# Performance work log

Hardware: AMD Instinct MI355X
Metric: run time of the kernel (lower is better)

## Reference

```python
import jax, jax.numpy as jnp
import numpy as np

N = 100000   # nodes
E = 1000000  # edges
G = 5000     # graphs
IN = 64; H = 64; ED = 16; OUT = 1
NUM_LAYERS = 3; NUM_TIMESTEPS = 2
SLOPE = 0.01

if NUM_LAYERS >= NUM_TIMESTEPS:
    CACHED_INDEX = list(range(-NUM_TIMESTEPS, 0))
else:
    CACHED_INDEX = list(range(-NUM_LAYERS, 0)) + [-1] * (NUM_TIMESTEPS - NUM_LAYERS)


def leaky(x):
    return jnp.where(x > 0, x, SLOPE * x)


def seg_softmax(scores, index, num_segments):
    # scores: [E] edge scores, softmax within segments given by index (PyG softmax, +1e-16 denom)
    m = jax.ops.segment_max(scores, index, num_segments)
    m = jnp.where(jnp.isfinite(m), m, 0.0)
    e = jnp.exp(scores - m[index])
    s = jax.ops.segment_sum(e, index, num_segments)
    return e / (s[index] + 1e-16)


def gru_cell(x, h, wih, whh, bih, bhh):
    # torch.nn.GRUCell math
    gi = x @ wih.T + bih
    gh = h @ whh.T + bhh
    ir, iz, inn = jnp.split(gi, 3, axis=-1)
    hr, hz, hn = jnp.split(gh, 3, axis=-1)
    r = jax.nn.sigmoid(ir + hr)
    z = jax.nn.sigmoid(iz + hz)
    n = jnp.tanh(inn + r * hn)
    return (1.0 - z) * n + z * h


def setup_inputs() -> dict:
    key = jax.random.key(0)
    ks = jax.random.split(key, 32)
    f32 = jnp.float32
    def w(k, shape, fan_in):
        return jax.random.normal(k, shape, f32) * (1.0 / np.sqrt(fan_in))
    L2 = NUM_LAYERS - 1
    inp = {}
    inp['raw'] = jax.random.normal(ks[0], (N, IN), f32)
    inp['edge_index'] = jax.random.randint(ks[1], (2, E), 0, N)
    inp['edge_attr'] = jax.random.normal(ks[2], (E, ED), f32)
    inp['batch'] = jnp.sort(jax.random.randint(ks[3], (N,), 0, G))
    inp['lin1_w'] = w(ks[4], (H, IN), IN); inp['lin1_b'] = jnp.zeros((H,), f32)
    inp['gate_nl_w'] = w(ks[5], (H, IN + ED), IN + ED); inp['gate_nl_b'] = jnp.zeros((H,), f32)
    inp['gate_align_w'] = w(ks[6], (1, 2 * H), 2 * H); inp['gate_align_b'] = jnp.zeros((1,), f32)
    inp['gate_attend_w'] = w(ks[7], (H, H), H); inp['gate_attend_b'] = jnp.zeros((H,), f32)
    inp['conv_align_w'] = w(ks[8], (L2, 1, 2 * H), 2 * H); inp['conv_align_b'] = jnp.zeros((L2, 1), f32)
    inp['conv_attend_w'] = w(ks[9], (L2, H, H), H); inp['conv_attend_b'] = jnp.zeros((L2, H), f32)
    inp['atom_gru_wih'] = w(ks[10], (NUM_LAYERS, 3 * H, H), H)
    inp['atom_gru_whh'] = w(ks[11], (NUM_LAYERS, 3 * H, H), H)
    inp['atom_gru_bih'] = jnp.zeros((NUM_LAYERS, 3 * H), f32)
    inp['atom_gru_bhh'] = jnp.zeros((NUM_LAYERS, 3 * H), f32)
    inp['mol_align_w'] = w(ks[12], (1, 2 * H), 2 * H); inp['mol_align_b'] = jnp.zeros((1,), f32)
    inp['mol_attend_w'] = w(ks[13], (H, H), H); inp['mol_attend_b'] = jnp.zeros((H,), f32)
    inp['mol_gru_wih'] = w(ks[14], (3 * H, H), H)
    inp['mol_gru_whh'] = w(ks[15], (3 * H, H), H)
    inp['mol_gru_bih'] = jnp.zeros((3 * H,), f32)
    inp['mol_gru_bhh'] = jnp.zeros((3 * H,), f32)
    inp['lin2_w'] = w(ks[16], (OUT, H), H); inp['lin2_b'] = jnp.zeros((OUT,), f32)
    return inp


def reference(raw, edge_index, edge_attr, batch,
              lin1_w, lin1_b,
              gate_nl_w, gate_nl_b, gate_align_w, gate_align_b, gate_attend_w, gate_attend_b,
              conv_align_w, conv_align_b, conv_attend_w, conv_attend_b,
              atom_gru_wih, atom_gru_whh, atom_gru_bih, atom_gru_bhh,
              mol_align_w, mol_align_b, mol_attend_w, mol_attend_b,
              mol_gru_wih, mol_gru_whh, mol_gru_bih, mol_gru_bhh,
              lin2_w, lin2_b):
    src, dst = edge_index[0], edge_index[1]
    x = leaky(raw @ lin1_w.T + lin1_b)  # [N, H]

    # --- GATEConv (layer 0): x_j from raw, x_i from x ---
    xj = leaky(jnp.concatenate([raw[src], edge_attr], axis=-1) @ gate_nl_w.T + gate_nl_b)  # [E, H]
    score = leaky(jnp.concatenate([x[dst], xj], axis=-1) @ gate_align_w.T + gate_align_b)  # [E, 1]
    aw = seg_softmax(score[:, 0], dst, N)[:, None]
    msg = (xj @ gate_attend_w.T + gate_attend_b) * aw
    h = jax.nn.elu(jax.ops.segment_sum(msg, dst, N))
    x = jax.nn.relu(gru_cell(h, x, atom_gru_wih[0], atom_gru_whh[0], atom_gru_bih[0], atom_gru_bhh[0]))
    cached = [x]

    # --- GATConv layers 1..L-1 ---
    for l in range(NUM_LAYERS - 1):
        xi, xj = x[dst], x[src]
        score = leaky(jnp.concatenate([xi, xj], axis=-1) @ conv_align_w[l].T + conv_align_b[l])
        aw = seg_softmax(score[:, 0], dst, N)[:, None]
        msg = (xj @ conv_attend_w[l].T + conv_attend_b[l]) * aw
        h = jax.nn.elu(jax.ops.segment_sum(msg, dst, N))
        x = jax.nn.relu(gru_cell(h, x, atom_gru_wih[l + 1], atom_gru_whh[l + 1],
                                 atom_gru_bih[l + 1], atom_gru_bhh[l + 1]))
        cached.append(x)

    # --- molecule-level readout ---
    out = jax.nn.relu(jax.ops.segment_sum(x, batch, G))  # [G, H]
    for t in range(NUM_TIMESTEPS):
        mixed = (x + cached[CACHED_INDEX[t]]) * 0.5  # [N, H] (x_j); x_i = out[batch]
        score = leaky(jnp.concatenate([out[batch], mixed], axis=-1) @ mol_align_w.T + mol_align_b)
        aw = seg_softmax(score[:, 0], batch, G)[:, None]
        msg = (mixed @ mol_attend_w.T + mol_attend_b) * aw
        h = jax.nn.elu(jax.ops.segment_sum(msg, batch, G))
        out = jax.nn.relu(gru_cell(h, out, mol_gru_wih, mol_gru_whh, mol_gru_bih, mol_gru_bhh))

    return out @ lin2_w.T + lin2_b  # [G, OUT]
```

## Files before the change

kernel.cpp:

```cpp
#include <hip/hip_runtime.h>
#include <math.h>

#define NPAD 65

__device__ __forceinline__ float leaky(float x) { return x > 0.f ? x : 0.01f * x; }
__device__ __forceinline__ float eluf(float x)  { return x > 0.f ? x : (__expf(x) - 1.f); }
__device__ __forceinline__ float sigm(float x)  { return 1.f / (1.f + __expf(-x)); }
__device__ __forceinline__ float tanhfast(float x) { return 1.f - 2.f / (__expf(2.f * x) + 1.f); }

__device__ __forceinline__ float bcastf(float v, int k) {
    return __uint_as_float((unsigned)__builtin_amdgcn_readlane((int)__float_as_uint(v), k));
}
__device__ __forceinline__ int bcasti(int v, int k) {
    return __builtin_amdgcn_readlane(v, k);
}
__device__ __forceinline__ float wredsum(float v) {
    #pragma unroll
    for (int off = 32; off; off >>= 1) v += __shfl_xor(v, off);
    return v;
}
__device__ __forceinline__ float wredmax(float v) {
    #pragma unroll
    for (int off = 32; off; off >>= 1) v = fmaxf(v, __shfl_xor(v, off));
    return v;
}

__global__ __launch_bounds__(256) void k_hist(const int* __restrict__ ei, int* __restrict__ deg, int E_) {
    int e = blockIdx.x * 256 + threadIdx.x;
    if (e < E_) atomicAdd(&deg[ei[E_ + e]], 1);
}

__global__ __launch_bounds__(256) void k_scan1(const int* __restrict__ deg, int* __restrict__ bsum, int N_) {
    __shared__ int s[256];
    int i = blockIdx.x * 256 + threadIdx.x;
    s[threadIdx.x] = (i < N_) ? deg[i] : 0;
    __syncthreads();
    for (int off = 128; off; off >>= 1) {
        if (threadIdx.x < off) s[threadIdx.x] += s[threadIdx.x + off];
        __syncthreads();
    }
    if (threadIdx.x == 0) bsum[blockIdx.x] = s[0];
}

__global__ __launch_bounds__(512) void k_scan2(int* __restrict__ bsum, int nb) {
    __shared__ int s[512];
    __shared__ int carry_s;
    if (threadIdx.x == 0) carry_s = 0;
    __syncthreads();
    for (int base = 0; base < nb; base += 512) {
        int t = threadIdx.x;
        int idx = base + t;
        int v = (idx < nb) ? bsum[idx] : 0;
        s[t] = v;
        __syncthreads();
        #pragma unroll
        for (int off = 1; off < 512; off <<= 1) {
            int u = (t >= off) ? s[t - off] : 0;
            __syncthreads();
            s[t] += u;
            __syncthreads();
        }
        int carry = carry_s;
        if (idx < nb) bsum[idx] = carry + s[t] - v;
        __syncthreads();
        if (t == 0) carry_s = carry + s[511];
        __syncthreads();
    }
}

__global__ __launch_bounds__(256) void k_scan3(const int* __restrict__ deg, const int* __restrict__ bsum,
                                               int* __restrict__ row, int* __restrict__ cur, int N_, int E_) {
    __shared__ int s[256];
    int i = blockIdx.x * 256 + threadIdx.x;
    int d = (i < N_) ? deg[i] : 0;
    s[threadIdx.x] = d;
    __syncthreads();
    for (int off = 1; off < 256; off <<= 1) {
        int v = (threadIdx.x >= off) ? s[threadIdx.x - off] : 0;
        __syncthreads();
        s[threadIdx.x] += v;
        __syncthreads();
    }
    if (i < N_) {
        int ex = bsum[blockIdx.x] + s[threadIdx.x] - d;
        row[i] = ex; cur[i] = ex;
    }
    if (i == N_ - 1) row[N_] = E_;
}

__global__ __launch_bounds__(256) void k_scatter(const int* __restrict__ ei, int* __restrict__ cur,
                                                 int* __restrict__ csrc, int* __restrict__ ceid, int E_) {
    int e = blockIdx.x * 256 + threadIdx.x;
    if (e >= E_) return;
    int dst = ei[E_ + e];
    int slot = atomicAdd(&cur[dst], 1);
    csrc[slot] = ei[e];
    ceid[slot] = e;
}

__global__ __launch_bounds__(256) void k_gbounds(const int* __restrict__ batch, int* __restrict__ gst,
                                                 int N_, int G_) {
    int i = blockIdx.x * 256 + threadIdx.x;
    if (i >= N_) return;
    int b = batch[i];
    int prev = (i == 0) ? -1 : batch[i - 1];
    for (int g = prev + 1; g <= b; ++g) gst[g] = i;
    if (i == N_ - 1) { for (int g = b + 1; g <= G_; ++g) gst[g] = N_; }
}

__global__ __launch_bounds__(256) void k_dense64(
    const float* __restrict__ in, const float* __restrict__ w, int wstride,
    const float* __restrict__ b, float* __restrict__ outp, int M, int act)
{
    __shared__ float ti[64 * NPAD];
    __shared__ float to[64 * NPAD];
    int r0 = blockIdx.x * 64;
    for (int i = threadIdx.x; i < 4096; i += 256) {
        int r = i >> 6, c = i & 63; int gr = r0 + r;
        ti[r * NPAD + c] = (gr < M) ? in[(size_t)gr * 64 + c] : 0.f;
    }
    __syncthreads();
    int n = threadIdx.x & 63;
    int jl = __builtin_amdgcn_readfirstlane((threadIdx.x >> 6) << 4);
    float acc[16];
    #pragma unroll
    for (int jj = 0; jj < 16; ++jj) acc[jj] = b[jl + jj];
    for (int kc = 0; kc < 64; kc += 16) {
        float xr[16];
        #pragma unroll
        for (int i = 0; i < 16; ++i) xr[i] = ti[n * NPAD + kc + i];
        #pragma unroll
        for (int jj = 0; jj < 16; ++jj) {
            const float* wr = w + (jl + jj) * wstride + kc;
            #pragma unroll
            for (int i = 0; i < 16; ++i) acc[jj] = fmaf(wr[i], xr[i], acc[jj]);
        }
    }
    #pragma unroll
    for (int jj = 0; jj < 16; ++jj) {
        float v = acc[jj];
        to[n * NPAD + jl + jj] = act ? leaky(v) : v;
    }
    __syncthreads();
    for (int i = threadIdx.x; i < 4096; i += 256) {
        int r = i >> 6, c = i & 63; int gr = r0 + r;
        if (gr < M) outp[(size_t)gr * 64 + c] = to[r * NPAD + c];
    }
}

__global__ __launch_bounds__(256) void k_node_dot2(
    const float* __restrict__ x, const float* __restrict__ wa,
    const float* __restrict__ wb, float* __restrict__ s,
    float* __restrict__ t, int n, int two)
{
    int gt = blockIdx.x * 256 + threadIdx.x;
    int wid = gt >> 6, lane = threadIdx.x & 63;
    if (wid >= n) return;
    float xv = x[(size_t)wid * 64 + lane];
    float a = xv * wa[lane];
    float bb = two ? xv * wb[lane] : 0.f;
    #pragma unroll
    for (int off = 32; off; off >>= 1) {
        a  += __shfl_down(a, off);
        bb += __shfl_down(bb, off);
    }
    if (lane == 0) { s[wid] = a; if (two) t[wid] = bb; }
}

#define GDOT(acc, A0, A1, A2, A3) \
    acc = fmaf(A0.x, w2[0], acc);  acc = fmaf(A0.y, w2[1], acc);  \
    acc = fmaf(A0.z, w2[2], acc);  acc = fmaf(A0.w, w2[3], acc);  \
    acc = fmaf(A1.x, w2[4], acc);  acc = fmaf(A1.y, w2[5], acc);  \
    acc = fmaf(A1.z, w2[6], acc);  acc = fmaf(A1.w, w2[7], acc);  \
    acc = fmaf(A2.x, w2[8], acc);  acc = fmaf(A2.y, w2[9], acc);  \
    acc = fmaf(A2.z, w2[10], acc); acc = fmaf(A2.w, w2[11], acc); \
    acc = fmaf(A3.x, w2[12], acc); acc = fmaf(A3.y, w2[13], acc); \
    acc = fmaf(A3.z, w2[14], acc); acc = fmaf(A3.w, w2[15], acc);

__global__ __launch_bounds__(256, 4) void k_gate_gather(
    const float* __restrict__ u, const float* __restrict__ ea,
    const int* __restrict__ row, const int* __restrict__ csrc, const int* __restrict__ ceid,
    const float* __restrict__ wnl,
    const float* __restrict__ gaw, const float* __restrict__ gab,
    const float* __restrict__ sarr, float* __restrict__ Agg, int N_)
{
    int wid = (blockIdx.x * 256 + threadIdx.x) >> 6;
    int lane = threadIdx.x & 63;
    if (wid >= N_) return;
    float w2[16];
    #pragma unroll
    for (int k = 0; k < 16; ++k) w2[k] = wnl[lane * 80 + 64 + k];
    float g2 = gaw[64 + lane];
    float gb = gab[0];
    float sdst = sarr[wid];
    int beg = row[wid], end = row[wid + 1];
    float m = -INFINITY, d = 0.f, S = 0.f;
    for (int cs = beg; cs < end; cs += 64) {
        int cnt = min(64, end - cs);
        int src_l = 0, eid_l = 0;
        if (lane < cnt) { src_l = csrc[cs + lane]; eid_l = ceid[cs + lane]; }
        int cnt2 = (cnt + 1) & ~1;
        int j1 = (1 < cnt) ? 1 : 0;
        int s0 = bcasti(src_l, 0), s1 = bcasti(src_l, j1);
        int e0 = bcasti(eid_l, 0), e1 = bcasti(eid_l, j1);
        float u0 = u[(size_t)s0 * 64 + lane];
        float u1 = u[(size_t)s1 * 64 + lane];
        const float4* p0 = (const float4*)(ea + (size_t)e0 * 16);
        const float4* p1 = (const float4*)(ea + (size_t)e1 * 16);
        float4 a00 = p0[0], a01 = p0[1], a02 = p0[2], a03 = p0[3];
        float4 a10 = p1[0], a11 = p1[1], a12 = p1[2], a13 = p1[3];
        for (int l = 0; l < cnt2; l += 2) {
            int ln0 = (l + 2 < cnt) ? l + 2 : l;
            int ln1 = (l + 3 < cnt) ? l + 3 : l;
            int ns0 = bcasti(src_l, ln0), ns1 = bcasti(src_l, ln1);
            int ne0 = bcasti(eid_l, ln0), ne1 = bcasti(eid_l, ln1);
            float nu0 = u[(size_t)ns0 * 64 + lane];
            float nu1 = u[(size_t)ns1 * 64 + lane];
            const float4* q0 = (const float4*)(ea + (size_t)ne0 * 16);
            const float4* q1 = (const float4*)(ea + (size_t)ne1 * 16);
            float4 b00 = q0[0], b01 = q0[1], b02 = q0[2], b03 = q0[3];
            float4 b10 = q1[0], b11 = q1[1], b12 = q1[2], b13 = q1[3];
            float acc0 = u0, acc1 = u1;
            GDOT(acc0, a00, a01, a02, a03)
            GDOT(acc1, a10, a11, a12, a13)
            float xj0 = leaky(acc0), xj1 = leaky(acc1);
            float t0 = xj0 * g2, t1 = xj1 * g2;
            #pragma unroll
            for (int off = 32; off; off >>= 1) {
                t0 += __shfl_xor(t0, off);
                t1 += __shfl_xor(t1, off);
            }
            float sc0 = leaky(sdst + t0 + gb);
            float sc1 = (l + 1 < cnt) ? leaky(sdst + t1 + gb) : -INFINITY;
            float mn = fmaxf(m, fmaxf(sc0, sc1));
            float c = __expf(m - mn);
            float q0e = __expf(sc0 - mn), q1e = __expf(sc1 - mn);
            S = S * c;
            S = fmaf(q0e, xj0, S); S = fmaf(q1e, xj1, S);
            d = d * c + (q0e + q1e);
            m = mn;
            u0 = nu0; u1 = nu1;
            a00 = b00; a01 = b01; a02 = b02; a03 = b03;
            a10 = b10; a11 = b11; a12 = b12; a13 = b13;
        }
    }
    Agg[(size_t)wid * 64 + lane] = S / (d + 1e-16f);
}

__global__ __launch_bounds__(256) void k_gat_gather(
    const int* __restrict__ row, const int* __restrict__ csrc,
    const float* __restrict__ x, const float* __restrict__ sarr,
    const float* __restrict__ tarr, const float* __restrict__ cb,
    float* __restrict__ Agg, int N_)
{
    int wid = (blockIdx.x * 256 + threadIdx.x) >> 6;
    int lane = threadIdx.x & 63;
    if (wid >= N_) return;
    float sdst = sarr[wid];
    float cbv = cb[0];
    int beg = row[wid], end = row[wid + 1];
    float m = -INFINITY, d = 0.f, S = 0.f;
    for (int cs = beg; cs < end; cs += 64) {
        int cnt = min(64, end - cs);
        int src_l = 0;
        if (lane < cnt) src_l = csrc[cs + lane];
        int s0 = bcasti(src_l, 0), s1 = bcasti(src_l, 1);
        int s2 = bcasti(src_l, 2), s3 = bcasti(src_l, 3);
        float r0 = x[(size_t)s0 * 64 + lane];
        float r1 = x[(size_t)s1 * 64 + lane];
        float r2 = x[(size_t)s2 * 64 + lane];
        float r3 = x[(size_t)s3 * 64 + lane];
        float sc_l = -INFINITY;
        if (lane < cnt) sc_l = leaky(sdst + tarr[src_l] + cbv);
        float cmax = wredmax(sc_l);
        float mn = fmaxf(m, cmax);
        float c = __expf(m - mn);
        float w_l = __expf(sc_l - mn);
        d = d * c + wredsum(w_l);
        S *= c;
        int cnt4 = (cnt + 3) & ~3;
        for (int l = 0; l < cnt4; l += 4) {
            int ln = (l + 4 < cnt4) ? l + 4 : 0;
            int t0 = bcasti(src_l, ln),     t1 = bcasti(src_l, ln + 1);
            int t2 = bcasti(src_l, ln + 2), t3 = bcasti(src_l, ln + 3);
            float p0 = x[(size_t)t0 * 64 + lane];
            float p1 = x[(size_t)t1 * 64 + lane];
            float p2 = x[(size_t)t2 * 64 + lane];
            float p3 = x[(size_t)t3 * 64 + lane];
            float w0 = bcastf(w_l, l),     w1 = bcastf(w_l, l + 1);
            float w2 = bcastf(w_l, l + 2), w3 = bcastf(w_l, l + 3);
            S = fmaf(w0, r0, S); S = fmaf(w1, r1, S);
            S = fmaf(w2, r2, S); S = fmaf(w3, r3, S);
            r0 = p0; r1 = p1; r2 = p2; r3 = p3;
        }
        m = mn;
    }
    Agg[(size_t)wid * 64 + lane] = S / (d + 1e-16f);
}

__global__ __launch_bounds__(512, 4) void k_node_update(
    const float* __restrict__ agg, const float* __restrict__ xold,
    const float* __restrict__ wa, const float* __restrict__ ba,
    const float* __restrict__ wih, const float* __restrict__ whh,
    const float* __restrict__ bih, const float* __restrict__ bhh,
    float* __restrict__ xout, int M,
    const float* __restrict__ dwa, const float* __restrict__ dwb,
    float* __restrict__ sout, float* __restrict__ tout)
{
    __shared__ float tA[128 * NPAD];
    __shared__ float tX[128 * NPAD];
    int r0 = blockIdx.x * 128;
    for (int j = threadIdx.x; j < 2048; j += 512) {
        int r = j >> 4, c4 = (j & 15) << 2; int gr = r0 + r;
        float4 av = make_float4(0.f, 0.f, 0.f, 0.f), xv = av;
        if (gr < M) {
            av = *(const float4*)(agg  + (size_t)gr * 64 + c4);
            xv = *(const float4*)(xold + (size_t)gr * 64 + c4);
        }
        int b = r * NPAD + c4;
        tA[b] = av.x; tA[b + 1] = av.y; tA[b + 2] = av.z; tA[b + 3] = av.w;
        tX[b] = xv.x; tX[b + 1] = xv.y; tX[b + 2] = xv.z; tX[b + 3] = xv.w;
    }
    __syncthreads();
    int n = threadIdx.x & 63;
    int jl = __builtin_amdgcn_readfirstlane((threadIdx.x >> 6) << 3);

    float hvA[8], hvB[8];
    {
        float accA[8], accB[8];
        #pragma unroll
        for (int jj = 0; jj < 8; ++jj) { float bv = ba[jl + jj]; accA[jj] = bv; accB[jj] = bv; }
        for (int kc = 0; kc < 64; kc += 16) {
            float aA[16], aB[16];
            #pragma unroll
            for (int i = 0; i < 16; ++i) {
                aA[i] = tA[n * NPAD + kc + i];
                aB[i] = tA[(n + 64) * NPAD + kc + i];
            }
            #pragma unroll
            for (int jj = 0; jj < 8; ++jj) {
                const float* wr = wa + (jl + jj) * 64 + kc;
                #pragma unroll
                for (int i = 0; i < 16; ++i) {
                    float wv = wr[i];
                    accA[jj] = fmaf(wv, aA[i], accA[jj]);
                    accB[jj] = fmaf(wv, aB[i], accB[jj]);
                }
            }
        }
        #pragma unroll
        for (int jj = 0; jj < 8; ++jj) { hvA[jj] = eluf(accA[jj]); hvB[jj] = eluf(accB[jj]); }
    }
    __syncthreads();
    #pragma unroll
    for (int jj = 0; jj < 8; ++jj) {
        tA[n * NPAD + jl + jj] = hvA[jj];
        tA[(n + 64) * NPAD + jl + jj] = hvB[jj];
    }
    __syncthreads();

    float rAc[8], rBc[8], zAc[8], zBc[8], nAc[8], nBc[8], hAc[8], hBc[8];
    #pragma unroll
    for (int jj = 0; jj < 8; ++jj) {
        float brz = bih[jl + jj] + bhh[jl + jj];
        float bz  = bih[64 + jl + jj] + bhh[64 + jl + jj];
        rAc[jj] = brz; rBc[jj] = brz;
        zAc[jj] = bz;  zBc[jj] = bz;
        nAc[jj] = bih[128 + jl + jj]; nBc[jj] = nAc[jj];
        hAc[jj] = bhh[128 + jl + jj]; hBc[jj] = hAc[jj];
    }
    for (int kc = 0; kc < 64; kc += 8) {
        float h0[8], h1[8], x0[8], x1[8];
        #pragma unroll
        for (int i = 0; i < 8; ++i) {
            h0[i] = tA[n * NPAD + kc + i];
            h1[i] = tA[(n + 64) * NPAD + kc + i];
            x0[i] = tX[n * NPAD + kc + i];
            x1[i] = tX[(n + 64) * NPAD + kc + i];
        }
        #pragma unroll
        for (int jj = 0; jj < 8; ++jj) {
            const float* w1 = wih + (jl + jj) * 64 + kc;
            const float* w4 = whh + (jl + jj) * 64 + kc;
            const float* w2 = wih + (64 + jl + jj) * 64 + kc;
            const float* w5 = whh + (64 + jl + jj) * 64 + kc;
            const float* w3 = wih + (128 + jl + jj) * 64 + kc;
            const float* w6 = whh + (128 + jl + jj) * 64 + kc;
            #pragma unroll
            for (int i = 0; i < 8; ++i) {
                float v1 = w1[i], v4 = w4[i], v2 = w2[i];
                float v5 = w5[i], v3 = w3[i], v6 = w6[i];
                rAc[jj] = fmaf(v1, h0[i], rAc[jj]); rAc[jj] = fmaf(v4, x0[i], rAc[jj]);
                rBc[jj] = fmaf(v1, h1[i], rBc[jj]); rBc[jj] = fmaf(v4, x1[i], rBc[jj]);
                zAc[jj] = fmaf(v2, h0[i], zAc[jj]); zAc[jj] = fmaf(v5, x0[i], zAc[jj]);
                zBc[jj] = fmaf(v2, h1[i], zBc[jj]); zBc[jj] = fmaf(v5, x1[i], zBc[jj]);
                nAc[jj] = fmaf(v3, h0[i], nAc[jj]); hAc[jj] = fmaf(v6, x0[i], hAc[jj]);
                nBc[jj] = fmaf(v3, h1[i], nBc[jj]); hBc[jj] = fmaf(v6, x1[i], hBc[jj]);
            }
        }
    }
    #pragma unroll
    for (int jj = 0; jj < 8; ++jj) {
        float r = sigm(rAc[jj]);
        float z = sigm(zAc[jj]);
        float nn = tanhfast(nAc[jj] + r * hAc[jj]);
        float xo = tX[n * NPAD + jl + jj];
        float v = (1.f - z) * nn + z * xo;
        hvA[jj] = fmaxf(v, 0.f);

        float rb = sigm(rBc[jj]);
        float zb = sigm(zBc[jj]);
        float nb_ = tanhfast(nBc[jj] + rb * hBc[jj]);
        float xob = tX[(n + 64) * NPAD + jl + jj];
        float vb = (1.f - zb) * nb_ + zb * xob;
        hvB[jj] = fmaxf(vb, 0.f);
    }
    __syncthreads();
    #pragma unroll
    for (int jj = 0; jj < 8; ++jj) {
        tA[n * NPAD + jl + jj] = hvA[jj];
        tA[(n + 64) * NPAD + jl + jj] = hvB[jj];
    }
    if (sout != nullptr) {
        float paA = 0.f, pbA = 0.f, paB = 0.f, pbB = 0.f;
        #pragma unroll
        for (int jj = 0; jj < 8; ++jj) {
            float wav = dwa[jl + jj], wbv = dwb[jl + jj];
            paA = fmaf(hvA[jj], wav, paA); pbA = fmaf(hvA[jj], wbv, pbA);
            paB = fmaf(hvB[jj], wav, paB); pbB = fmaf(hvB[jj], wbv, pbB);
        }
        int w2i = (threadIdx.x >> 6) << 1;
        tX[n * 17 + w2i]            = paA;
        tX[n * 17 + w2i + 1]        = pbA;
        tX[(n + 64) * 17 + w2i]     = paB;
        tX[(n + 64) * 17 + w2i + 1] = pbB;
    }
    __syncthreads();
    for (int j = threadIdx.x; j < 2048; j += 512) {
        int r = j >> 4, c4 = (j & 15) << 2; int gr = r0 + r;
        if (gr < M) {
            int b = r * NPAD + c4;
            float4 ov = make_float4(tA[b], tA[b + 1], tA[b + 2], tA[b + 3]);
            *(float4*)(xout + (size_t)gr * 64 + c4) = ov;
        }
    }
    if (sout != nullptr && threadIdx.x < 128) {
        int r = threadIdx.x; int gr = r0 + r;
        if (gr < M) {
            float sa = 0.f, sb = 0.f;
            #pragma unroll
            for (int w = 0; w < 16; w += 2) { sa += tX[r * 17 + w]; sb += tX[r * 17 + w + 1]; }
            sout[gr] = sa; tout[gr] = sb;
        }
    }
}

__global__ __launch_bounds__(256) void k_seg_sum_relu(
    const float* __restrict__ x, const int* __restrict__ gst,
    float* __restrict__ outp, int G_)
{
    int g = (blockIdx.x * 256 + threadIdx.x) >> 6;
    int lane = threadIdx.x & 63;
    if (g >= G_) return;
    float S0 = 0.f, S1 = 0.f, S2 = 0.f, S3 = 0.f;
    int end = gst[g + 1];
    int i = gst[g];
    for (; i + 4 <= end; i += 4) {
        S0 += x[(size_t)i * 64 + lane];
        S1 += x[(size_t)(i + 1) * 64 + lane];
        S2 += x[(size_t)(i + 2) * 64 + lane];
        S3 += x[(size_t)(i + 3) * 64 + lane];
    }
    for (; i < end; ++i) S0 += x[(size_t)i * 64 + lane];
    outp[(size_t)g * 64 + lane] = fmaxf((S0 + S1) + (S2 + S3), 0.f);
}

__global__ __launch_bounds__(256) void k_mol_dots(
    const float* __restrict__ xf, const float* __restrict__ cach,
    const float* __restrict__ maw, float* __restrict__ dd, int n)
{
    int wid = (blockIdx.x * 256 + threadIdx.x) >> 6;
    int lane = threadIdx.x & 63;
    if (wid >= n) return;
    float mix = 0.5f * (xf[(size_t)wid * 64 + lane] + cach[(size_t)wid * 64 + lane]);
    float v = wredsum(mix * maw[64 + lane]);
    if (lane == 0) dd[wid] = v;
}

__global__ __launch_bounds__(256) void k_mol_gather(
    const float* __restrict__ xf, const float* __restrict__ cach,
    const float* __restrict__ stateIn, const int* __restrict__ gst,
    const float* __restrict__ dd,
    const float* __restrict__ maw, const float* __restrict__ mab,
    float* __restrict__ Agg, int G_)
{
    int g = (blockIdx.x * 256 + threadIdx.x) >> 6;
    int lane = threadIdx.x & 63;
    if (g >= G_) return;
    float o = stateIn[(size_t)g * 64 + lane];
    float og = wredsum(o * maw[lane]);
    float mb = mab[0];
    int beg = gst[g], end = gst[g + 1];
    float m = -INFINITY, d = 0.f, S = 0.f;
    for (int cs = beg; cs < end; cs += 64) {
        int cnt = min(64, end - cs);
        size_t rb = (size_t)cs * 64 + lane;
        float x0 = xf[rb],      c0 = cach[rb];
        float x1 = xf[rb + 64], c1 = cach[rb + 64];
        float x2 = xf[rb + 128], c2 = cach[rb + 128];
        float x3 = xf[rb + 192], c3 = cach[rb + 192];
        float sc_l = -INFINITY;
        if (lane < cnt) sc_l = leaky(og + dd[cs + lane] + mb);
        float cmax = wredmax(sc_l);
        float mn = fmaxf(m, cmax);
        float c = __expf(m - mn);
        float w_l = __expf(sc_l - mn);
        d = d * c + wredsum(w_l);
        S *= c;
        int cnt4 = (cnt + 3) & ~3;
        for (int l = 0; l < cnt4; l += 4) {
            int ln = (l + 4 < cnt4) ? l + 4 : 0;
            size_t rn = (size_t)(cs + ln) * 64 + lane;
            float y0 = xf[rn],       d0 = cach[rn];
            float y1 = xf[rn + 64],  d1 = cach[rn + 64];
            float y2 = xf[rn + 128], d2 = cach[rn + 128];
            float y3 = xf[rn + 192], d3 = cach[rn + 192];
            float w0 = bcastf(w_l, l),     w1 = bcastf(w_l, l + 1);
            float w2 = bcastf(w_l, l + 2), w3 = bcastf(w_l, l + 3);
            S = fmaf(w0, 0.5f * (x0 + c0), S);
            S = fmaf(w1, 0.5f * (x1 + c1), S);
            S = fmaf(w2, 0.5f * (x2 + c2), S);
            S = fmaf(w3, 0.5f * (x3 + c3), S);
            x0 = y0; c0 = d0; x1 = y1; c1 = d1;
            x2 = y2; c2 = d2; x3 = y3; c3 = d3;
        }
        m = mn;
    }
    Agg[(size_t)g * 64 + lane] = S / (d + 1e-16f);
}

__global__ __launch_bounds__(256) void k_lin2(
    const float* __restrict__ st, const float* __restrict__ w,
    const float* __restrict__ b, float* __restrict__ outp, int g)
{
    int gt = blockIdx.x * 256 + threadIdx.x;
    int wid = gt >> 6, lane = threadIdx.x & 63;
    if (wid >= g) return;
    float v = st[(size_t)wid * 64 + lane] * w[lane];
    #pragma unroll
    for (int off = 32; off; off >>= 1) v += __shfl_down(v, off);
    if (lane == 0) outp[wid] = v + b[0];
}

extern "C" void kernel_launch(void* const* d_in, const int* in_sizes, int n_in,
                              void* d_out, int out_size, void* d_ws, size_t ws_size,
                              hipStream_t stream) {
    const float* raw           = (const float*)d_in[0];
    const int*   ei            = (const int*)d_in[1];
    const float* ea            = (const float*)d_in[2];
    const int*   batch         = (const int*)d_in[3];
    const float* lin1_w        = (const float*)d_in[4];
    const float* lin1_b        = (const float*)d_in[5];
    const float* gate_nl_w     = (const float*)d_in[6];
    const float* gate_nl_b     = (const float*)d_in[7];
    const float* gate_align_w  = (const float*)d_in[8];
    const float* gate_align_b  = (const float*)d_in[9];
    const float* gate_attend_w = (const float*)d_in[10];
    const float* gate_attend_b = (const float*)d_in[11];
    const float* conv_align_w  = (const float*)d_in[12];
    const float* conv_align_b  = (const float*)d_in[13];
    const float* conv_attend_w = (const float*)d_in[14];
    const float* conv_attend_b = (const float*)d_in[15];
    const float* gru_wih       = (const float*)d_in[16];
    const float* gru_whh       = (const float*)d_in[17];
    const float* gru_bih       = (const float*)d_in[18];
    const float* gru_bhh       = (const float*)d_in[19];
    const float* mol_align_w   = (const float*)d_in[20];
    const float* mol_align_b   = (const float*)d_in[21];
    const float* mol_attend_w  = (const float*)d_in[22];
    const float* mol_attend_b  = (const float*)d_in[23];
    const float* mol_wih       = (const float*)d_in[24];
    const float* mol_whh       = (const float*)d_in[25];
    const float* mol_bih       = (const float*)d_in[26];
    const float* mol_bhh       = (const float*)d_in[27];
    const float* lin2_w        = (const float*)d_in[28];
    const float* lin2_b        = (const float*)d_in[29];
    float* out = (float*)d_out;

    const int N = in_sizes[3];
    const int E = in_sizes[1] / 2;
    const int G = out_size;
    const size_t N64 = (size_t)N * 64;
    const size_t G64 = (size_t)G * 64;

    float* f = (float*)d_ws;
    float* xA    = f;
    float* xB    = xA + N64;
    float* xD    = xB + N64;
    float* Agg   = xD + N64;
    float* u     = Agg + N64;
    float* sN    = u + N64;
    float* tN    = sN + N;
    float* dd    = tN + N;
    float* outS  = dd + N;
    float* outS2 = outS + G64;
    float* aggG  = outS2 + G64;
    int* row  = (int*)(aggG + G64);
    int* csrc = row + (N + 1);
    int* ceid = csrc + E;
    int* bsum = ceid + E;
    int* gst  = bsum + 512;
    int* deg = (int*)Agg;
    int* cur = deg + N;

    const int nb_node64  = (N + 63) / 64;
    const int nb_node128 = (N + 127) / 128;
    const int nb_edge   = (E + 255) / 256;
    const int nb_nodes  = (N + 255) / 256;
    const int nb_waveN  = (N + 3) / 4;
    const int nb_waveG  = (G + 3) / 4;
    const int nb_nodeG  = (G + 127) / 128;

    hipMemsetAsync(deg, 0, (size_t)N * 4, stream);
    k_hist<<<nb_edge, 256, 0, stream>>>(ei, deg, E);
    k_scan1<<<nb_nodes, 256, 0, stream>>>(deg, bsum, N);
    k_scan2<<<1, 512, 0, stream>>>(bsum, nb_nodes);
    k_scan3<<<nb_nodes, 256, 0, stream>>>(deg, bsum, row, cur, N, E);
    k_scatter<<<nb_edge, 256, 0, stream>>>(ei, cur, csrc, ceid, E);
    k_gbounds<<<nb_nodes, 256, 0, stream>>>(batch, gst, N, G);

    k_dense64<<<nb_node64, 256, 0, stream>>>(raw, lin1_w, 64, lin1_b, xA, N, 1);
    k_dense64<<<nb_node64, 256, 0, stream>>>(raw, gate_nl_w, 80, gate_nl_b, u, N, 0);

    k_node_dot2<<<nb_waveN, 256, 0, stream>>>(xA, gate_align_w, gate_align_w, sN, tN, N, 0);
    k_gate_gather<<<nb_waveN, 256, 0, stream>>>(u, ea, row, csrc, ceid,
                                                gate_nl_w, gate_align_w, gate_align_b,
                                                sN, Agg, N);
    k_node_update<<<nb_node128, 512, 0, stream>>>(Agg, xA, gate_attend_w, gate_attend_b,
                                                  gru_wih, gru_whh, gru_bih, gru_bhh, xB, N,
                                                  conv_align_w, conv_align_w + 64, sN, tN);

    k_gat_gather<<<nb_waveN, 256, 0, stream>>>(row, csrc, xB, sN, tN, conv_align_b, Agg, N);
    k_node_update<<<nb_node128, 512, 0, stream>>>(Agg, xB, conv_attend_w, conv_attend_b,
                                                  gru_wih + 12288, gru_whh + 12288,
                                                  gru_bih + 192, gru_bhh + 192, xD, N,
                                                  conv_align_w + 128, conv_align_w + 192, sN, tN);

    k_gat_gather<<<nb_waveN, 256, 0, stream>>>(row, csrc, xD, sN, tN, conv_align_b + 1, Agg, N);
    k_node_update<<<nb_node128, 512, 0, stream>>>(Agg, xD, conv_attend_w + 4096, conv_attend_b + 64,
                                                  gru_wih + 24576, gru_whh + 24576,
                                                  gru_bih + 384, gru_bhh + 384, xA, N,
                                                  nullptr, nullptr, nullptr, nullptr);

    k_seg_sum_relu<<<nb_waveG, 256, 0, stream>>>(xA, gst, outS, G);

    const float* cachedP[2] = { xD, xA };
    float* sIn = outS; float* sOut = outS2;
    for (int t = 0; t < 2; ++t) {
        k_mol_dots<<<nb_waveN, 256, 0, stream>>>(xA, cachedP[t], mol_align_w, dd, N);
        k_mol_gather<<<nb_waveG, 256, 0, stream>>>(xA, cachedP[t], sIn, gst, dd,
                                                   mol_align_w, mol_align_b, aggG, G);
        k_node_update<<<nb_nodeG, 512, 0, stream>>>(aggG, sIn, mol_attend_w, mol_attend_b,
                                                    mol_wih, mol_whh, mol_bih, mol_bhh, sOut, G,
                                                    nullptr, nullptr, nullptr, nullptr);
        float* tmp = sIn; sIn = sOut; sOut = tmp;
    }

    k_lin2<<<nb_waveG, 256, 0, stream>>>(sIn, lin2_w, lin2_b, out, G);
}
```

Measured before the change: 1.091 ms.

## Fuse node dot products and final linear into producer kernel epilogues

```diff
diff --git a/kernel.cpp b/kernel.cpp
--- a/kernel.cpp
+++ b/kernel.cpp
@@ -110,7 +110,8 @@
 
 __global__ __launch_bounds__(256) void k_dense64(
     const float* __restrict__ in, const float* __restrict__ w, int wstride,
-    const float* __restrict__ b, float* __restrict__ outp, int M, int act)
+    const float* __restrict__ b, float* __restrict__ outp, int M, int act,
+    const float* __restrict__ dva, float* __restrict__ dsout)
 {
     __shared__ float ti[64 * NPAD];
     __shared__ float to[64 * NPAD];
@@ -146,25 +147,16 @@
         int r = i >> 6, c = i & 63; int gr = r0 + r;
         if (gr < M) outp[(size_t)gr * 64 + c] = to[r * NPAD + c];
     }
-}
-
-__global__ __launch_bounds__(256) void k_node_dot2(
-    const float* __restrict__ x, const float* __restrict__ wa,
-    const float* __restrict__ wb, float* __restrict__ s,
-    float* __restrict__ t, int n, int two)
-{
-    int gt = blockIdx.x * 256 + threadIdx.x;
-    int wid = gt >> 6, lane = threadIdx.x & 63;
-    if (wid >= n) return;
-    float xv = x[(size_t)wid * 64 + lane];
-    float a = xv * wa[lane];
-    float bb = two ? xv * wb[lane] : 0.f;
-    #pragma unroll
-    for (int off = 32; off; off >>= 1) {
-        a  += __shfl_down(a, off);
-        bb += __shfl_down(bb, off);
-    }
-    if (lane == 0) { s[wid] = a; if (two) t[wid] = bb; }
+    if (dsout != nullptr) {
+        int wv = threadIdx.x >> 6;
+        float wval = dva[n];
+        #pragma unroll 4
+        for (int q = 0; q < 16; ++q) {
+            int r = (wv << 4) + q; int gr = r0 + r;
+            float pv = wredsum(to[r * NPAD + n] * wval);
+            if (n == 0 && gr < M) dsout[gr] = pv;
+        }
+    }
 }
 
 #define GDOT(acc, A0, A1, A2, A3) \
@@ -305,7 +297,7 @@
     const float* __restrict__ bih, const float* __restrict__ bhh,
     float* __restrict__ xout, int M,
     const float* __restrict__ dwa, const float* __restrict__ dwb,
-    float* __restrict__ sout, float* __restrict__ tout)
+    float* __restrict__ sout, float* __restrict__ tout, int mode)
 {
     __shared__ float tA[128 * NPAD];
     __shared__ float tX[128 * NPAD];
@@ -399,6 +391,7 @@
             }
         }
     }
+    float paA = 0.f, pbA = 0.f, paB = 0.f, pbB = 0.f;
     #pragma unroll
     for (int jj = 0; jj < 8; ++jj) {
         float r = sigm(rAc[jj]);
@@ -414,6 +407,15 @@
         float xob = tX[(n + 64) * NPAD + jl + jj];
         float vb = (1.f - zb) * nb_ + zb * xob;
         hvB[jj] = fmaxf(vb, 0.f);
+
+        if (sout != nullptr) {
+            float wav = dwa[jl + jj];
+            float wbv = (mode == 0) ? dwb[jl + jj] : wav;
+            float a1A = (mode == 1) ? 0.5f * (hvA[jj] + xo)  : hvA[jj];
+            float a1B = (mode == 1) ? 0.5f * (hvB[jj] + xob) : hvB[jj];
+            paA = fmaf(a1A, wav, paA); pbA = fmaf(hvA[jj], wbv, pbA);
+            paB = fmaf(a1B, wav, paB); pbB = fmaf(hvB[jj], wbv, pbB);
+        }
     }
     __syncthreads();
     #pragma unroll
@@ -422,13 +424,6 @@
         tA[(n + 64) * NPAD + jl + jj] = hvB[jj];
     }
     if (sout != nullptr) {
-        float paA = 0.f, pbA = 0.f, paB = 0.f, pbB = 0.f;
-        #pragma unroll
-        for (int jj = 0; jj < 8; ++jj) {
-            float wav = dwa[jl + jj], wbv = dwb[jl + jj];
-            paA = fmaf(hvA[jj], wav, paA); pbA = fmaf(hvA[jj], wbv, pbA);
-            paB = fmaf(hvB[jj], wav, paB); pbB = fmaf(hvB[jj], wbv, pbB);
-        }
         int w2i = (threadIdx.x >> 6) << 1;
         tX[n * 17 + w2i]            = paA;
         tX[n * 17 + w2i + 1]        = pbA;
@@ -450,7 +445,11 @@
             float sa = 0.f, sb = 0.f;
             #pragma unroll
             for (int w = 0; w < 16; w += 2) { sa += tX[r * 17 + w]; sb += tX[r * 17 + w + 1]; }
-            sout[gr] = sa; tout[gr] = sb;
+            if (mode == 2) {
+                sout[gr] = sa + dwb[0];
+            } else {
+                sout[gr] = sa; tout[gr] = sb;
+            }
         }
     }
 }
@@ -473,18 +472,6 @@
     }
     for (; i < end; ++i) S0 += x[(size_t)i * 64 + lane];
     outp[(size_t)g * 64 + lane] = fmaxf((S0 + S1) + (S2 + S3), 0.f);
-}
-
-__global__ __launch_bounds__(256) void k_mol_dots(
-    const float* __restrict__ xf, const float* __restrict__ cach,
-    const float* __restrict__ maw, float* __restrict__ dd, int n)
-{
-    int wid = (blockIdx.x * 256 + threadIdx.x) >> 6;
-    int lane = threadIdx.x & 63;
-    if (wid >= n) return;
-    float mix = 0.5f * (xf[(size_t)wid * 64 + lane] + cach[(size_t)wid * 64 + lane]);
-    float v = wredsum(mix * maw[64 + lane]);
-    if (lane == 0) dd[wid] = v;
 }
 
 __global__ __launch_bounds__(256) void k_mol_gather(
@@ -539,19 +526,6 @@
     Agg[(size_t)g * 64 + lane] = S / (d + 1e-16f);
 }
 
-__global__ __launch_bounds__(256) void k_lin2(
-    const float* __restrict__ st, const float* __restrict__ w,
-    const float* __restrict__ b, float* __restrict__ outp, int g)
-{
-    int gt = blockIdx.x * 256 + threadIdx.x;
-    int wid = gt >> 6, lane = threadIdx.x & 63;
-    if (wid >= g) return;
-    float v = st[(size_t)wid * 64 + lane] * w[lane];
-    #pragma unroll
-    for (int off = 32; off; off >>= 1) v += __shfl_down(v, off);
-    if (lane == 0) outp[wid] = v + b[0];
-}
-
 extern "C" void kernel_launch(void* const* d_in, const int* in_sizes, int n_in,
                               void* d_out, int out_size, void* d_ws, size_t ws_size,
                               hipStream_t stream) {
@@ -629,42 +603,40 @@
     k_scatter<<<nb_edge, 256, 0, stream>>>(ei, cur, csrc, ceid, E);
     k_gbounds<<<nb_nodes, 256, 0, stream>>>(batch, gst, N, G);
 
-    k_dense64<<<nb_node64, 256, 0, stream>>>(raw, lin1_w, 64, lin1_b, xA, N, 1);
-    k_dense64<<<nb_node64, 256, 0, stream>>>(raw, gate_nl_w, 80, gate_nl_b, u, N, 0);
-
-    k_node_dot2<<<nb_waveN, 256, 0, stream>>>(xA, gate_align_w, gate_align_w, sN, tN, N, 0);
+    k_dense64<<<nb_node64, 256, 0, stream>>>(raw, lin1_w, 64, lin1_b, xA, N, 1,
+                                             gate_align_w, sN);
+    k_dense64<<<nb_node64, 256, 0, stream>>>(raw, gate_nl_w, 80, gate_nl_b, u, N, 0,
+                                             nullptr, nullptr);
+
     k_gate_gather<<<nb_waveN, 256, 0, stream>>>(u, ea, row, csrc, ceid,
                                                 gate_nl_w, gate_align_w, gate_align_b,
                                                 sN, Agg, N);
     k_node_update<<<nb_node128, 512, 0, stream>>>(Agg, xA, gate_attend_w, gate_attend_b,
                                                   gru_wih, gru_whh, gru_bih, gru_bhh, xB, N,
-                                                  conv_align_w, conv_align_w + 64, sN, tN);
+                                                  conv_align_w, conv_align_w + 64, sN, tN, 0);
 
     k_gat_gather<<<nb_waveN, 256, 0, stream>>>(row, csrc, xB, sN, tN, conv_align_b, Agg, N);
     k_node_update<<<nb_node128, 512, 0, stream>>>(Agg, xB, conv_attend_w, conv_attend_b,
                                                   gru_wih + 12288, gru_whh + 12288,
                                                   gru_bih + 192, gru_bhh + 192, xD, N,
-                                                  conv_align_w + 128, conv_align_w + 192, sN, tN);
+                                                  conv_align_w + 128, conv_align_w + 192, sN, tN, 0);
 
     k_gat_gather<<<nb_waveN, 256, 0, stream>>>(row, csrc, xD, sN, tN, conv_align_b + 1, Agg, N);
     k_node_update<<<nb_node128, 512, 0, stream>>>(Agg, xD, conv_attend_w + 4096, conv_attend_b + 64,
                                                   gru_wih + 24576, gru_whh + 24576,
                                                   gru_bih + 384, gru_bhh + 384, xA, N,
-                                                  nullptr, nullptr, nullptr, nullptr);
+                                                  mol_align_w + 64, mol_align_w + 64, dd, tN, 1);
 
     k_seg_sum_relu<<<nb_waveG, 256, 0, stream>>>(xA, gst, outS, G);
 
-    const float* cachedP[2] = { xD, xA };
-    float* sIn = outS; float* sOut = outS2;
-    for (int t = 0; t < 2; ++t) {
-        k_mol_dots<<<nb_waveN, 256, 0, stream>>>(xA, cachedP[t], mol_align_w, dd, N);
-        k_mol_gather<<<nb_waveG, 256, 0, stream>>>(xA, cachedP[t], sIn, gst, dd,
-                                                   mol_align_w, mol_align_b, aggG, G);
-        k_node_update<<<nb_nodeG, 512, 0, stream>>>(aggG, sIn, mol_attend_w, mol_attend_b,
-                                                    mol_wih, mol_whh, mol_bih, mol_bhh, sOut, G,
-                                                    nullptr, nullptr, nullptr, nullptr);
-        float* tmp = sIn; sIn = sOut; sOut = tmp;
-    }
-
-    k_lin2<<<nb_waveG, 256, 0, stream>>>(sIn, lin2_w, lin2_b, out, G);
-}
+    k_mol_gather<<<nb_waveG, 256, 0, stream>>>(xA, xD, outS, gst, dd,
+                                               mol_align_w, mol_align_b, aggG, G);
+    k_node_update<<<nb_nodeG, 512, 0, stream>>>(aggG, outS, mol_attend_w, mol_attend_b,
+                                                mol_wih, mol_whh, mol_bih, mol_bhh, outS2, G,
+                                                nullptr, nullptr, nullptr, nullptr, 0);
+    k_mol_gather<<<nb_waveG, 256, 0, stream>>>(xA, xA, outS2, gst, tN,
+                                               mol_align_w, mol_align_b, aggG, G);
+    k_node_update<<<nb_nodeG, 512, 0, stream>>>(aggG, outS2, mol_attend_w, mol_attend_b,
+                                                mol_wih, mol_whh, mol_bih, mol_bhh, outS, G,
+                                                lin2_w, lin2_b, out, nullptr, 2);
+}
```

New measurement: 1.071 ms. Within noise of the previous version (-1.8%).
